# Kernel tuning notes

Measured on AMD Instinct MI355X. Metric: run time of the kernel, lower is better.

## Reference

```python
import jax, jax.numpy as jnp
import numpy as np

N_PANO, N_FP = 50000, 10000
D_IN, D_FP, HID, OUT = 128, 64, 128, 64
E_PP, E_PF = 800000, 50000


def _gat(x_src, x_dst, src, dst, Ws, Wd, a_s, a_d, b, n_dst):
    # PyG GATConv (heads=1, add_self_loops=False, bipartite lin_src/lin_dst)
    hs = x_src @ Ws                      # [Ns, C]
    hd = x_dst @ Wd                      # [Nd, C]
    es = hs @ a_s                        # [Ns]
    ed = hd @ a_d                        # [Nd]
    e = jax.nn.leaky_relu(es[src] + ed[dst], negative_slope=0.2)  # [E]
    m = jax.ops.segment_max(e, dst, num_segments=n_dst)
    ex = jnp.exp(e - m[dst])
    den = jax.ops.segment_sum(ex, dst, num_segments=n_dst)
    alpha = ex / den[dst]                # segment softmax over incoming edges
    out = jax.ops.segment_sum(hs[src] * alpha[:, None], dst, num_segments=n_dst)
    return out + b


def setup_inputs() -> dict:
    key = jax.random.key(0)
    ks = jax.random.split(key, 32)
    s_in = 1.0 / np.sqrt(D_IN)
    s_hid = 1.0 / np.sqrt(HID)
    s_fp = 1.0 / np.sqrt(D_FP)
    inp = {
        "x_pano": jax.random.normal(ks[0], (N_PANO, D_IN), jnp.float32),
        "x_fp": jax.random.normal(ks[1], (N_FP, D_FP), jnp.float32),
        # layer 0 (in = D_IN)
        "Ws0": jax.random.normal(ks[2], (D_IN, HID)) * s_in,
        "Wd0": jax.random.normal(ks[3], (D_IN, HID)) * s_in,
        "as0": jax.random.normal(ks[4], (HID,)) * 0.1,
        "ad0": jax.random.normal(ks[5], (HID,)) * 0.1,
        "b0": jnp.zeros((HID,), jnp.float32),
        "Lw0": jax.random.normal(ks[6], (D_IN, HID)) * s_in,
        "Lb0": jnp.zeros((HID,), jnp.float32),
        # layer 1 (in = HID)
        "Ws1": jax.random.normal(ks[7], (HID, HID)) * s_hid,
        "Wd1": jax.random.normal(ks[8], (HID, HID)) * s_hid,
        "as1": jax.random.normal(ks[9], (HID,)) * 0.1,
        "ad1": jax.random.normal(ks[10], (HID,)) * 0.1,
        "b1": jnp.zeros((HID,), jnp.float32),
        "Lw1": jax.random.normal(ks[11], (HID, HID)) * s_hid,
        "Lb1": jnp.zeros((HID,), jnp.float32),
        # translate conv pano -> footprint
        "Wts": jax.random.normal(ks[12], (HID, OUT)) * s_hid,
        "Wtd": jax.random.normal(ks[13], (D_FP, OUT)) * s_fp,
        "ats": jax.random.normal(ks[14], (OUT,)) * 0.1,
        "atd": jax.random.normal(ks[15], (OUT,)) * 0.1,
        "bt": jnp.zeros((OUT,), jnp.float32),
        "edge_pp": jax.random.randint(ks[16], (2, E_PP), 0, N_PANO),
        "edge_pf_src": jax.random.randint(ks[17], (E_PF,), 0, N_PANO),
        "edge_pf_dst": jax.random.randint(ks[18], (E_PF,), 0, N_FP),
    }
    return inp


def reference(x_pano, x_fp, Ws0, Wd0, as0, ad0, b0, Lw0, Lb0,
              Ws1, Wd1, as1, ad1, b1, Lw1, Lb1,
              Wts, Wtd, ats, atd, bt,
              edge_pp, edge_pf_src, edge_pf_dst):
    src, dst = edge_pp[0], edge_pp[1]
    layer_params = [(Ws0, Wd0, as0, ad0, b0, Lw0, Lb0),
                    (Ws1, Wd1, as1, ad1, b1, Lw1, Lb1)]
    h = x_pano
    for (Ws, Wd, a_s, a_d, b, Lw, Lb) in layer_params:
        conv = _gat(h, h, src, dst, Ws, Wd, a_s, a_d, b, N_PANO)
        h = jax.nn.relu(conv + h @ Lw + Lb)
    # HeteroConv with single relation + aggr='sum' == the bipartite conv output
    out_fp = _gat(h, x_fp, edge_pf_src, edge_pf_dst, Wts, Wtd, ats, atd, bt, N_FP)
    return out_fp
```

## Files before the change

kernel.cpp:

```cpp
#include <hip/hip_runtime.h>
#include <hip/hip_bf16.h>
#include <math.h>

#define N_PANO 50000
#define N_FP   10000
#define N_UNI  60000
#define HID    128
#define OUT_C  64
#define E_PP   800000
#define E_PF   50000
#define E_UNI  850000
#define NBKT   235
#define EPB    4096

typedef unsigned short ushort_t;
typedef unsigned int uint_t;
typedef __attribute__((ext_vector_type(8))) short short8;
typedef __attribute__((ext_vector_type(4))) float f32x4;

static inline int cdiv(int a, int b) { return (a + b - 1) / b; }

__device__ inline ushort_t f2bf(float x) {
    __hip_bfloat16 h = __float2bfloat16(x);
    return *reinterpret_cast<ushort_t*>(&h);
}
__device__ inline float bfu2f(ushort_t u) {
    return __uint_as_float(((uint_t)u) << 16);
}
__device__ inline float bflo(uint_t u) { return __uint_as_float((u & 0xffffu) << 16); }
__device__ inline float bfhi(uint_t u) { return __uint_as_float(u & 0xffff0000u); }
__device__ inline f32x4 mfma16(short8 a, short8 b, f32x4 c) {
    return __builtin_amdgcn_mfma_f32_16x16x32_bf16(a, b, c, 0, 0, 0);
}

__global__ __launch_bounds__(256) void zero_i32(int* p, int n) {
    int i = blockIdx.x * 256 + threadIdx.x;
    if (i < n) p[i] = 0;
}

__global__ __launch_bounds__(256) void bucket_count(const int* __restrict__ pp_dst,
                                                    const int* __restrict__ pf_dst,
                                                    int* __restrict__ bcnt) {
    __shared__ int hist[NBKT];
    const int tid = threadIdx.x;
    const int e0 = blockIdx.x * EPB;
    for (int t = tid; t < NBKT; t += 256) hist[t] = 0;
    __syncthreads();
    #pragma unroll
    for (int u = 0; u < EPB / 256; ++u) {
        int e = e0 + u * 256 + tid;
        int d = -1;
        if (e < E_PP) d = pp_dst[e];
        else if (e < E_UNI) d = N_PANO + pf_dst[e - E_PP];
        if (d >= 0) atomicAdd(&hist[d >> 8], 1);
    }
    __syncthreads();
    for (int t = tid; t < NBKT; t += 256)
        if (hist[t] > 0) atomicAdd(&bcnt[t * 16], hist[t]);
}

__global__ __launch_bounds__(256) void bucket_scan(const int* __restrict__ bcnt,
                                                   int* __restrict__ base, int* __restrict__ bcur) {
    __shared__ int wsum[4];
    int tid = threadIdx.x, lane = tid & 63, wid = tid >> 6;
    int v = (tid < NBKT) ? bcnt[tid * 16] : 0;
    int incl = v;
    #pragma unroll
    for (int off = 1; off < 64; off <<= 1) {
        int t = __shfl_up(incl, off, 64);
        if (lane >= off) incl += t;
    }
    if (lane == 63) wsum[wid] = incl;
    __syncthreads();
    if (tid == 0) {
        int run = 0;
        #pragma unroll
        for (int w = 0; w < 4; ++w) { int t = wsum[w]; wsum[w] = run; run += t; }
    }
    __syncthreads();
    int excl = wsum[wid] + incl - v;
    if (tid < NBKT) { base[tid] = excl; bcur[tid * 16] = excl; }
    if (tid == NBKT) base[NBKT] = E_UNI;
}

__global__ __launch_bounds__(256) void bucket_scatter_uni(const int* __restrict__ pp_src,
                                                          const int* __restrict__ pp_dst,
                                                          const int* __restrict__ pf_src,
                                                          const int* __restrict__ pf_dst,
                                                          int* __restrict__ bcur, int2* __restrict__ tmp) {
    __shared__ int hist[NBKT];
    __shared__ int base[NBKT];
    const int tid = threadIdx.x;
    const int e0 = blockIdx.x * EPB;
    for (int t = tid; t < NBKT; t += 256) hist[t] = 0;
    __syncthreads();
    int d[16], s[16];
    #pragma unroll
    for (int u = 0; u < 16; ++u) {
        int e = e0 + u * 256 + tid;
        if (e < E_PP)       { d[u] = pp_dst[e];                 s[u] = pp_src[e]; }
        else if (e < E_UNI) { d[u] = N_PANO + pf_dst[e - E_PP]; s[u] = pf_src[e - E_PP]; }
        else d[u] = -1;
        if (d[u] >= 0) atomicAdd(&hist[d[u] >> 8], 1);
    }
    __syncthreads();
    for (int t = tid; t < NBKT; t += 256) {
        int c = hist[t];
        base[t] = (c > 0) ? atomicAdd(&bcur[t * 16], c) : 0;
        hist[t] = 0;
    }
    __syncthreads();
    #pragma unroll
    for (int u = 0; u < 16; ++u) {
        if (d[u] >= 0) {
            int b = d[u] >> 8;
            int p = base[b] + atomicAdd(&hist[b], 1);
            tmp[p] = make_int2(s[u], d[u]);
        }
    }
}

__global__ __launch_bounds__(256) void bucket_fine_sort(const int2* __restrict__ tmp,
                                                        const int* __restrict__ base,
                                                        int* __restrict__ ptr, int* __restrict__ col) {
    __shared__ int hist[256];
    __shared__ int wsum[4];
    const int b = blockIdx.x, tid = threadIdx.x, lane = tid & 63, wid = tid >> 6;
    const int B0 = base[b], B1 = base[b + 1];
    hist[tid] = 0;
    __syncthreads();
    for (int e = B0 + tid; e < B1; e += 256) atomicAdd(&hist[tmp[e].y & 255], 1);
    __syncthreads();
    int v = hist[tid];
    int incl = v;
    #pragma unroll
    for (int off = 1; off < 64; off <<= 1) {
        int t = __shfl_up(incl, off, 64);
        if (lane >= off) incl += t;
    }
    if (lane == 63) wsum[wid] = incl;
    __syncthreads();
    if (tid == 0) {
        int run = 0;
        #pragma unroll
        for (int w = 0; w < 4; ++w) { int t = wsum[w]; wsum[w] = run; run += t; }
    }
    __syncthreads();
    int excl = wsum[wid] + incl - v;
    int dg = b * 256 + tid;
    if (dg < N_UNI) ptr[dg] = B0 + excl;
    if (b == NBKT - 1 && tid == 0) ptr[N_UNI] = E_UNI;
    hist[tid] = excl;
    __syncthreads();
    for (int e = B0 + tid; e < B1; e += 256) {
        int2 ed = tmp[e];
        int p = B0 + atomicAdd(&hist[ed.y & 255], 1);
        col[p] = ed.x;
    }
}

__global__ __launch_bounds__(256) void prep_k(const float* __restrict__ Ws0, const float* __restrict__ Lw0,
                                              const float* __restrict__ Ws1, const float* __restrict__ Lw1,
                                              const float* __restrict__ Wts,
                                              const float* __restrict__ Wd0, const float* __restrict__ ad0,
                                              const float* __restrict__ Wd1, const float* __restrict__ ad1,
                                              const float* __restrict__ Wtd, const float* __restrict__ atd,
                                              ushort_t* s0, ushort_t* l0, ushort_t* s1, ushort_t* l1,
                                              ushort_t* ts,
                                              float* wed0, float* wed1, float* wedt) {
    const int blk = blockIdx.x, tid = threadIdx.x;
    if (blk < 288) {
        int i = blk * 256 + tid;
        const float* W; ushort_t* oh;
        int d, NIc, Cc;
        if (i < 65536) {
            int m = i >> 14; d = i & 16383;
            W = (m == 0) ? Ws0 : (m == 1) ? Lw0 : (m == 2) ? Ws1 : Lw1;
            oh = (m == 0) ? s0 : (m == 1) ? l0 : (m == 2) ? s1 : l1;
            NIc = 8; Cc = 128;
        } else if (i < 73728) {
            d = i - 65536; W = Wts; oh = ts;
            NIc = 4; Cc = 64;
        } else return;
        int j = d & 7, l = (d >> 3) & 63;
        int kcl = (d >> 9) & 1;
        int ni = (d >> 10) & (NIc - 1);
        int p = d >> (10 + (NIc == 8 ? 3 : 2));
        int kc = p * 2 + kcl;
        int n = ni * 16 + (l & 15);
        int k = kc * 32 + (l >> 4) * 8 + j;
        oh[d] = f2bf(W[k * Cc + n]);
    } else {
        int r = (blk - 288) * 4 + (tid >> 6);
        int lane = tid & 63;
        const float* W; const float* a; float* o; int rr, C;
        if (r < 128)      { W = Wd0; a = ad0; o = wed0; rr = r;       C = 128; }
        else if (r < 256) { W = Wd1; a = ad1; o = wed1; rr = r - 128; C = 128; }
        else if (r < 320) { W = Wtd; a = atd; o = wedt; rr = r - 256; C = 64;  }
        else return;
        float s = 0.f;
        for (int j = lane; j < C; j += 64) s += W[rr * C + j] * a[j];
        #pragma unroll
        for (int off = 32; off; off >>= 1) s += __shfl_down(s, off, 64);
        if (lane == 0) o[rr] = s;
    }
}

template <int CN, bool DUAL, bool FP32IN>
__global__ __launch_bounds__(256, 2) void gemm_mfma(const float* __restrict__ Xf,
                                                 const ushort_t* __restrict__ Xh,
                                                 const ushort_t* __restrict__ W1, const ushort_t* __restrict__ W2,
                                                 ushort_t* __restrict__ Y1, ushort_t* __restrict__ Y2,
                                                 const float* __restrict__ avec, float* __restrict__ evec,
                                                 const float* __restrict__ wed, float* __restrict__ edv,
                                                 int N) {
    constexpr int NI = CN / 16;
    constexpr int NMAT = DUAL ? 2 : 1;
    constexpr int SLAB = NI * 1024;
    __shared__ ushort_t Bsh[NMAT * SLAB];
    const int tid = threadIdx.x;
    const int w = tid >> 6, l = tid & 63;
    const int col = l & 15, q = l >> 4;
    const int row0 = blockIdx.x * 128 + w * 32;
    f32x4 acc1[2][NI];
    f32x4 acc2[2][DUAL ? NI : 1];
    #pragma unroll
    for (int m = 0; m < 2; ++m)
        #pragma unroll
        for (int ni = 0; ni < NI; ++ni)
            #pragma unroll
            for (int r = 0; r < 4; ++r) acc1[m][ni][r] = 0.f;
    if (DUAL) {
        #pragma unroll
        for (int m = 0; m < 2; ++m)
            #pragma unroll
            for (int ni = 0; ni < NI; ++ni)
                #pragma unroll
                for (int r = 0; r < 4; ++r) acc2[m][ni][r] = 0.f;
    }
    float ped[2] = {0.f, 0.f};

    #pragma unroll
    for (int p = 0; p < 2; ++p) {
        if (p) __syncthreads();
        {
            const uint4* src1 = (const uint4*)W1 + p * (SLAB / 8);
            uint4* dst1 = (uint4*)&Bsh[0];
            #pragma unroll
            for (int f = tid; f < SLAB / 8; f += 256) dst1[f] = src1[f];
            if (DUAL) {
                const uint4* src2 = (const uint4*)W2 + p * (SLAB / 8);
                uint4* dst2 = (uint4*)&Bsh[SLAB];
                #pragma unroll
                for (int f = tid; f < SLAB / 8; f += 256) dst2[f] = src2[f];
            }
        }
        __syncthreads();
        #pragma unroll
        for (int kcl = 0; kcl < 2; ++kcl) {
            const int kc = p * 2 + kcl;
            const int k0 = kc * 32 + q * 8;
            short8 Ah[2];
            #pragma unroll
            for (int m = 0; m < 2; ++m) {
                const int arow = row0 + m * 16 + col;
                if (FP32IN) {
                    float xv[8];
                    if (arow < N) {
                        float4 a0 = *(const float4*)&Xf[(size_t)arow * 128 + k0];
                        float4 a1 = *(const float4*)&Xf[(size_t)arow * 128 + k0 + 4];
                        xv[0] = a0.x; xv[1] = a0.y; xv[2] = a0.z; xv[3] = a0.w;
                        xv[4] = a1.x; xv[5] = a1.y; xv[6] = a1.z; xv[7] = a1.w;
                    } else {
                        #pragma unroll
                        for (int j = 0; j < 8; ++j) xv[j] = 0.f;
                    }
                    #pragma unroll
                    for (int j = 0; j < 8; ++j) Ah[m][j] = (short)f2bf(xv[j]);
                    if (wed) {
                        float4 w0 = *(const float4*)&wed[k0];
                        float4 w1 = *(const float4*)&wed[k0 + 4];
                        ped[m] += xv[0] * w0.x + xv[1] * w0.y + xv[2] * w0.z + xv[3] * w0.w
                                + xv[4] * w1.x + xv[5] * w1.y + xv[6] * w1.z + xv[7] * w1.w;
                    }
                } else {
                    if (arow < N) {
                        Ah[m] = *(const short8*)&Xh[(size_t)arow * 128 + k0];
                    } else {
                        #pragma unroll
                        for (int j = 0; j < 8; ++j) Ah[m][j] = 0;
                    }
                    if (wed) {
                        float4 w0 = *(const float4*)&wed[k0];
                        float4 w1 = *(const float4*)&wed[k0 + 4];
                        float wv[8] = {w0.x, w0.y, w0.z, w0.w, w1.x, w1.y, w1.z, w1.w};
                        #pragma unroll
                        for (int j = 0; j < 8; ++j)
                            ped[m] += bfu2f((ushort_t)Ah[m][j]) * wv[j];
                    }
                }
            }
            #pragma unroll
            for (int ni = 0; ni < NI; ++ni) {
                const int lb = ((ni * 2 + kcl) * 64 + l) * 8;
                short8 B1 = *(const short8*)&Bsh[lb];
                #pragma unroll
                for (int m = 0; m < 2; ++m) acc1[m][ni] = mfma16(Ah[m], B1, acc1[m][ni]);
                if (DUAL) {
                    short8 B2 = *(const short8*)&Bsh[SLAB + lb];
                    #pragma unroll
                    for (int m = 0; m < 2; ++m) acc2[m][ni] = mfma16(Ah[m], B2, acc2[m][ni]);
                }
            }
        }
    }

    #pragma unroll
    for (int m = 0; m < 2; ++m) {
        #pragma unroll
        for (int ni = 0; ni < NI; ++ni) {
            #pragma unroll
            for (int r = 0; r < 4; ++r) {
                int mrow = row0 + m * 16 + q * 4 + r;
                if (mrow < N) {
                    Y1[(size_t)mrow * CN + ni * 16 + col] = f2bf(acc1[m][ni][r]);
                    if (DUAL) Y2[(size_t)mrow * CN + ni * 16 + col] = f2bf(acc2[m][ni][r]);
                }
            }
        }
    }
    float av[NI];
    #pragma unroll
    for (int ni = 0; ni < NI; ++ni) av[ni] = avec[ni * 16 + col];
    #pragma unroll
    for (int m = 0; m < 2; ++m) {
        #pragma unroll
        for (int r = 0; r < 4; ++r) {
            float pp = 0.f;
            #pragma unroll
            for (int ni = 0; ni < NI; ++ni) pp += acc1[m][ni][r] * av[ni];
            pp += __shfl_xor(pp, 1, 64);
            pp += __shfl_xor(pp, 2, 64);
            pp += __shfl_xor(pp, 4, 64);
            pp += __shfl_xor(pp, 8, 64);
            int mrow = row0 + m * 16 + q * 4 + r;
            if (col == 0 && mrow < N) evec[mrow] = pp;
        }
    }
    if (wed) {
        #pragma unroll
        for (int m = 0; m < 2; ++m) {
            ped[m] += __shfl_xor(ped[m], 16, 64);
            ped[m] += __shfl_xor(ped[m], 32, 64);
            int arow = row0 + m * 16 + col;
            if (q == 0 && arow < N) edv[arow] = ped[m];
        }
    }
}

__global__ __launch_bounds__(256) void agg_pano7(const int* __restrict__ ptr, const int* __restrict__ col,
                                                 const float* __restrict__ es, const float* __restrict__ ed,
                                                 const ushort_t* __restrict__ hsb, const ushort_t* __restrict__ linb,
                                                 const float* __restrict__ b, const float* __restrict__ Lb,
                                                 uint_t* __restrict__ hh, int N) {
    int lane = threadIdx.x & 63, wid = threadIdx.x >> 6;
    int nodeA = blockIdx.x * 8 + wid * 2;
    if (nodeA >= N) return;
    int nodeB = nodeA + 1;
    bool hasB = nodeB < N;
    int begA = ptr[nodeA], endA = ptr[nodeA + 1];
    int endB = hasB ? ptr[nodeB + 1] : endA;
    int begB = endA;
    float ednA = ed[nodeA];
    float ednB = hasB ? ed[nodeB] : 0.f;
    const int half = lane >> 5, hl = lane & 31;
    float aA0 = 0.f, aA1 = 0.f, aA2 = 0.f, aA3 = 0.f, dA = 0.f;
    float aB0 = 0.f, aB1 = 0.f, aB2 = 0.f, aB3 = 0.f, dB = 0.f;
    int baseA = begA, baseB = begB;
    while (baseA < endA || baseB < endB) {
        int mA = endA - baseA; mA = mA < 0 ? 0 : (mA > 64 ? 64 : mA);
        int mB = endB - baseB; mB = mB < 0 ? 0 : (mB > 64 ? 64 : mB);
        int sA = 0, sB = 0;
        float wA = 0.f, wB = 0.f;
        if (lane < mA) {
            sA = col[baseA + lane];
            float e = es[sA] + ednA;
            e = fmaxf(e, 0.2f * e);
            wA = __expf(e);
        }
        if (lane < mB) {
            sB = col[baseB + lane];
            float e = es[sB] + ednB;
            e = fmaxf(e, 0.2f * e);
            wB = __expf(e);
        }
        dA += wA; dB += wB;
        {
            int mp = (mA + 1) & ~1;
            int t = 0;
            for (; t + 8 <= mp; t += 8) {
                int i0 = t + half, i1 = t + 2 + half, i2 = t + 4 + half, i3 = t + 6 + half;
                int s0 = __shfl(sA, i0, 64), s1 = __shfl(sA, i1, 64);
                int s2 = __shfl(sA, i2, 64), s3 = __shfl(sA, i3, 64);
                float w0 = __shfl(wA, i0, 64), w1 = __shfl(wA, i1, 64);
                float w2 = __shfl(wA, i2, 64), w3 = __shfl(wA, i3, 64);
                uint2 h0 = *(const uint2*)&hsb[(size_t)s0 * 128 + hl * 4];
                uint2 h1 = *(const uint2*)&hsb[(size_t)s1 * 128 + hl * 4];
                uint2 h2 = *(const uint2*)&hsb[(size_t)s2 * 128 + hl * 4];
                uint2 h3 = *(const uint2*)&hsb[(size_t)s3 * 128 + hl * 4];
                aA0 += w0 * bflo(h0.x) + w1 * bflo(h1.x) + w2 * bflo(h2.x) + w3 * bflo(h3.x);
                aA1 += w0 * bfhi(h0.x) + w1 * bfhi(h1.x) + w2 * bfhi(h2.x) + w3 * bfhi(h3.x);
                aA2 += w0 * bflo(h0.y) + w1 * bflo(h1.y) + w2 * bflo(h2.y) + w3 * bflo(h3.y);
                aA3 += w0 * bfhi(h0.y) + w1 * bfhi(h1.y) + w2 * bfhi(h2.y) + w3 * bfhi(h3.y);
            }
            for (; t < mp; t += 2) {
                int i0 = t + half;
                int s0 = __shfl(sA, i0, 64);
                float w0 = __shfl(wA, i0, 64);
                uint2 h0 = *(const uint2*)&hsb[(size_t)s0 * 128 + hl * 4];
                aA0 += w0 * bflo(h0.x);
                aA1 += w0 * bfhi(h0.x);
                aA2 += w0 * bflo(h0.y);
                aA3 += w0 * bfhi(h0.y);
            }
        }
        {
            int mp = (mB + 1) & ~1;
            int t = 0;
            for (; t + 8 <= mp; t += 8) {
                int i0 = t + half, i1 = t + 2 + half, i2 = t + 4 + half, i3 = t + 6 + half;
                int s0 = __shfl(sB, i0, 64), s1 = __shfl(sB, i1, 64);
                int s2 = __shfl(sB, i2, 64), s3 = __shfl(sB, i3, 64);
                float w0 = __shfl(wB, i0, 64), w1 = __shfl(wB, i1, 64);
                float w2 = __shfl(wB, i2, 64), w3 = __shfl(wB, i3, 64);
                uint2 h0 = *(const uint2*)&hsb[(size_t)s0 * 128 + hl * 4];
                uint2 h1 = *(const uint2*)&hsb[(size_t)s1 * 128 + hl * 4];
                uint2 h2 = *(const uint2*)&hsb[(size_t)s2 * 128 + hl * 4];
                uint2 h3 = *(const uint2*)&hsb[(size_t)s3 * 128 + hl * 4];
                aB0 += w0 * bflo(h0.x) + w1 * bflo(h1.x) + w2 * bflo(h2.x) + w3 * bflo(h3.x);
                aB1 += w0 * bfhi(h0.x) + w1 * bfhi(h1.x) + w2 * bfhi(h2.x) + w3 * bfhi(h3.x);
                aB2 += w0 * bflo(h0.y) + w1 * bflo(h1.y) + w2 * bflo(h2.y) + w3 * bflo(h3.y);
                aB3 += w0 * bfhi(h0.y) + w1 * bfhi(h1.y) + w2 * bfhi(h2.y) + w3 * bfhi(h3.y);
            }
            for (; t < mp; t += 2) {
                int i0 = t + half;
                int s0 = __shfl(sB, i0, 64);
                float w0 = __shfl(wB, i0, 64);
                uint2 h0 = *(const uint2*)&hsb[(size_t)s0 * 128 + hl * 4];
                aB0 += w0 * bflo(h0.x);
                aB1 += w0 * bfhi(h0.x);
                aB2 += w0 * bflo(h0.y);
                aB3 += w0 * bfhi(h0.y);
            }
        }
        baseA += 64; baseB += 64;
    }
    aA0 += __shfl_xor(aA0, 32, 64); aA1 += __shfl_xor(aA1, 32, 64);
    aA2 += __shfl_xor(aA2, 32, 64); aA3 += __shfl_xor(aA3, 32, 64);
    aB0 += __shfl_xor(aB0, 32, 64); aB1 += __shfl_xor(aB1, 32, 64);
    aB2 += __shfl_xor(aB2, 32, 64); aB3 += __shfl_xor(aB3, 32, 64);
    #pragma unroll
    for (int off = 1; off < 64; off <<= 1) dA += __shfl_xor(dA, off, 64);
    #pragma unroll
    for (int off = 1; off < 64; off <<= 1) dB += __shfl_xor(dB, off, 64);
    float invA = (endA > begA) ? (1.f / dA) : 0.f;
    float invB = (endB > begB) ? (1.f / dB) : 0.f;
    int node = half ? nodeB : nodeA;
    if (half == 0 || hasB) {
        float v0 = half ? aB0 : aA0, v1 = half ? aB1 : aA1;
        float v2 = half ? aB2 : aA2, v3 = half ? aB3 : aA3;
        float inv = half ? invB : invA;
        uint2 lv = *(const uint2*)&linb[(size_t)node * 128 + hl * 4];
        float4 bb = *(const float4*)&b[hl * 4];
        float4 lb4 = *(const float4*)&Lb[hl * 4];
        float o0 = fmaxf(v0 * inv + bb.x + bflo(lv.x) + lb4.x, 0.f);
        float o1 = fmaxf(v1 * inv + bb.y + bfhi(lv.x) + lb4.y, 0.f);
        float o2 = fmaxf(v2 * inv + bb.z + bflo(lv.y) + lb4.z, 0.f);
        float o3 = fmaxf(v3 * inv + bb.w + bfhi(lv.y) + lb4.w, 0.f);
        uint2 ov;
        ov.x = (uint_t)f2bf(o0) | ((uint_t)f2bf(o1) << 16);
        ov.y = (uint_t)f2bf(o2) | ((uint_t)f2bf(o3) << 16);
        *(uint2*)&hh[(size_t)node * 64 + hl * 2] = ov;
    }
}

__global__ __launch_bounds__(256) void agg_fp5(const int* __restrict__ ptr, const int* __restrict__ col,
                                               const float* __restrict__ es, const float* __restrict__ x_fp,
                                               const float* __restrict__ wedt,
                                               const ushort_t* __restrict__ hsb, const float* __restrict__ bt,
                                               float* __restrict__ out, int N) {
    int lane = threadIdx.x & 63, wid = threadIdx.x >> 6;
    int node = blockIdx.x * 4 + wid;
    if (node >= N) return;
    int beg = ptr[node], end = ptr[node + 1];
    float edn = x_fp[(size_t)node * 64 + lane] * wedt[lane];
    #pragma unroll
    for (int off = 1; off < 64; off <<= 1) edn += __shfl_xor(edn, off, 64);
    float acc = 0.f, denp = 0.f;
    for (int base = beg; base < end; base += 64) {
        int m = min(64, end - base);
        int s = 0;
        float wgt = 0.f;
        if (lane < m) {
            s = col[base + lane];
            float e = es[s] + edn;
            e = fmaxf(e, 0.2f * e);
            wgt = __expf(e);
        }
        denp += wgt;
        int u = 0;
        for (; u + 4 <= m; u += 4) {
            int s0 = __shfl(s, u, 64), s1 = __shfl(s, u + 1, 64);
            int s2 = __shfl(s, u + 2, 64), s3 = __shfl(s, u + 3, 64);
            float w0 = __shfl(wgt, u, 64), w1 = __shfl(wgt, u + 1, 64);
            float w2 = __shfl(wgt, u + 2, 64), w3 = __shfl(wgt, u + 3, 64);
            float h0 = bfu2f(hsb[(size_t)s0 * 64 + lane]);
            float h1 = bfu2f(hsb[(size_t)s1 * 64 + lane]);
            float h2 = bfu2f(hsb[(size_t)s2 * 64 + lane]);
            float h3 = bfu2f(hsb[(size_t)s3 * 64 + lane]);
            acc += w0 * h0 + w1 * h1 + w2 * h2 + w3 * h3;
        }
        for (; u < m; ++u) {
            int su = __shfl(s, u, 64);
            float wu = __shfl(wgt, u, 64);
            acc += wu * bfu2f(hsb[(size_t)su * 64 + lane]);
        }
    }
    float den = denp;
    #pragma unroll
    for (int off = 1; off < 64; off <<= 1) den += __shfl_xor(den, off, 64);
    float inv = (end > beg) ? (1.f / den) : 0.f;
    out[(size_t)node * 64 + lane] = acc * inv + bt[lane];
}

extern "C" void kernel_launch(void* const* d_in, const int* in_sizes, int n_in,
                              void* d_out, int out_size, void* d_ws, size_t ws_size,
                              hipStream_t stream) {
    const float* x_pano = (const float*)d_in[0];
    const float* x_fp   = (const float*)d_in[1];
    const float* Ws0 = (const float*)d_in[2];
    const float* Wd0 = (const float*)d_in[3];
    const float* as0 = (const float*)d_in[4];
    const float* ad0 = (const float*)d_in[5];
    const float* b0  = (const float*)d_in[6];
    const float* Lw0 = (const float*)d_in[7];
    const float* Lb0 = (const float*)d_in[8];
    const float* Ws1 = (const float*)d_in[9];
    const float* Wd1 = (const float*)d_in[10];
    const float* as1 = (const float*)d_in[11];
    const float* ad1 = (const float*)d_in[12];
    const float* b1  = (const float*)d_in[13];
    const float* Lw1 = (const float*)d_in[14];
    const float* Lb1 = (const float*)d_in[15];
    const float* Wts = (const float*)d_in[16];
    const float* Wtd = (const float*)d_in[17];
    const float* ats = (const float*)d_in[18];
    const float* atd = (const float*)d_in[19];
    const float* bt  = (const float*)d_in[20];
    const int* edge_pp = (const int*)d_in[21];
    const int* pf_src  = (const int*)d_in[22];
    const int* pf_dst  = (const int*)d_in[23];
    float* out = (float*)d_out;

    char* wsp = (char*)d_ws;
    size_t off = 0;
    auto alloc = [&](size_t bytes) -> char* {
        char* p = wsp + off;
        off += (bytes + 255) & ~(size_t)255;
        return p;
    };
    ushort_t* hsb  = (ushort_t*)alloc(sizeof(ushort_t) * N_PANO * HID);
    ushort_t* linb = (ushort_t*)alloc(sizeof(ushort_t) * N_PANO * HID);
    uint_t* hh     = (uint_t*)alloc(sizeof(uint_t) * N_PANO * 64);
    ushort_t* hstb = (ushort_t*)alloc(sizeof(ushort_t) * N_PANO * OUT_C);
    int2* tmp_e    = (int2*)alloc(sizeof(int2) * E_UNI);
    float* es   = (float*)alloc(sizeof(float) * N_PANO);
    float* ed   = (float*)alloc(sizeof(float) * N_PANO);
    float* wed0 = (float*)alloc(sizeof(float) * HID);
    float* wed1 = (float*)alloc(sizeof(float) * HID);
    float* wedt = (float*)alloc(sizeof(float) * OUT_C);
    ushort_t* s0 = (ushort_t*)alloc(sizeof(ushort_t) * 128 * 128);
    ushort_t* l0 = (ushort_t*)alloc(sizeof(ushort_t) * 128 * 128);
    ushort_t* s1 = (ushort_t*)alloc(sizeof(ushort_t) * 128 * 128);
    ushort_t* l1 = (ushort_t*)alloc(sizeof(ushort_t) * 128 * 128);
    ushort_t* ts = (ushort_t*)alloc(sizeof(ushort_t) * 64 * 128);
    int* bcnt   = (int*)alloc(sizeof(int) * NBKT * 16);
    int* bcur   = (int*)alloc(sizeof(int) * NBKT * 16);
    int* bbase  = (int*)alloc(sizeof(int) * (NBKT + 1));
    int* P      = (int*)alloc(sizeof(int) * (N_UNI + 1));
    int* col_u  = (int*)alloc(sizeof(int) * E_UNI);

    const int* pp_src = edge_pp;
    const int* pp_dst = edge_pp + E_PP;

    zero_i32<<<cdiv(NBKT * 16, 256), 256, 0, stream>>>(bcnt, NBKT * 16);
    bucket_count<<<cdiv(E_UNI, EPB), 256, 0, stream>>>(pp_dst, pf_dst, bcnt);
    bucket_scan<<<1, 256, 0, stream>>>(bcnt, bbase, bcur);
    bucket_scatter_uni<<<cdiv(E_UNI, EPB), 256, 0, stream>>>(pp_src, pp_dst, pf_src, pf_dst, bcur, tmp_e);
    bucket_fine_sort<<<NBKT, 256, 0, stream>>>(tmp_e, bbase, P, col_u);

    prep_k<<<368, 256, 0, stream>>>(Ws0, Lw0, Ws1, Lw1, Wts, Wd0, ad0, Wd1, ad1, Wtd, atd,
                                    s0, l0, s1, l1, ts, wed0, wed1, wedt);

    const int gemm_grid = cdiv(N_PANO, 128);

    gemm_mfma<128, true, true><<<gemm_grid, 256, 0, stream>>>(
        x_pano, nullptr, s0, l0, hsb, linb, as0, es, wed0, ed, N_PANO);
    agg_pano7<<<cdiv(N_PANO, 8), 256, 0, stream>>>(P, col_u, es, ed, hsb, linb, b0, Lb0, hh, N_PANO);

    gemm_mfma<128, true, false><<<gemm_grid, 256, 0, stream>>>(
        nullptr, (const ushort_t*)hh, s1, l1, hsb, linb, as1, es, wed1, ed, N_PANO);
    agg_pano7<<<cdiv(N_PANO, 8), 256, 0, stream>>>(P, col_u, es, ed, hsb, linb, b1, Lb1, hh, N_PANO);

    gemm_mfma<64, false, false><<<gemm_grid, 256, 0, stream>>>(
        nullptr, (const ushort_t*)hh, ts, nullptr, hstb, nullptr, ats, es, nullptr, nullptr, N_PANO);
    agg_fp5<<<cdiv(N_FP, 4), 256, 0, stream>>>(P + N_PANO, col_u, es, x_fp, wedt, hstb, bt, out, N_FP);
}
```

Before: 277.8 us.

## Replace atomic bucket sort with per-tile counts, scan, and fused weight prep

Removes the zero kernel and the global atomic bucket cursors. Each edge tile now writes its per-bucket histogram to a tile-major count matrix, a per-bucket scan computes exclusive offsets, and the scatter places edges at fixed positions without global atomics. Weight conversion prep is folded into the count kernel launch. This cuts kernel launches from six to four, removes global atomic contention, and makes the coarse ordering deterministic. In exchange, the scatter re-scans bucket totals in every block.

Result: faster. 267.4 us (-3.7%).

```diff
diff --git a/kernel.cpp b/kernel.cpp
--- a/kernel.cpp
+++ b/kernel.cpp
@@ -12,6 +12,7 @@
 #define E_UNI  850000
 #define NBKT   235
 #define EPB    4096
+#define NT_CNT 208
 
 typedef unsigned short ushort_t;
 typedef unsigned int uint_t;
@@ -33,144 +34,35 @@
     return __builtin_amdgcn_mfma_f32_16x16x32_bf16(a, b, c, 0, 0, 0);
 }
 
-__global__ __launch_bounds__(256) void zero_i32(int* p, int n) {
-    int i = blockIdx.x * 256 + threadIdx.x;
-    if (i < n) p[i] = 0;
-}
-
-__global__ __launch_bounds__(256) void bucket_count(const int* __restrict__ pp_dst,
-                                                    const int* __restrict__ pf_dst,
-                                                    int* __restrict__ bcnt) {
+__global__ __launch_bounds__(256) void csr_count_prep(
+        const int* __restrict__ pp_dst, const int* __restrict__ pf_dst,
+        int* __restrict__ pcnt,
+        const float* __restrict__ Ws0, const float* __restrict__ Lw0,
+        const float* __restrict__ Ws1, const float* __restrict__ Lw1,
+        const float* __restrict__ Wts,
+        const float* __restrict__ Wd0, const float* __restrict__ ad0,
+        const float* __restrict__ Wd1, const float* __restrict__ ad1,
+        const float* __restrict__ Wtd, const float* __restrict__ atd,
+        ushort_t* s0, ushort_t* l0, ushort_t* s1, ushort_t* l1, ushort_t* ts,
+        float* wed0, float* wed1, float* wedt) {
     __shared__ int hist[NBKT];
-    const int tid = threadIdx.x;
-    const int e0 = blockIdx.x * EPB;
-    for (int t = tid; t < NBKT; t += 256) hist[t] = 0;
-    __syncthreads();
-    #pragma unroll
-    for (int u = 0; u < EPB / 256; ++u) {
-        int e = e0 + u * 256 + tid;
-        int d = -1;
-        if (e < E_PP) d = pp_dst[e];
-        else if (e < E_UNI) d = N_PANO + pf_dst[e - E_PP];
-        if (d >= 0) atomicAdd(&hist[d >> 8], 1);
-    }
-    __syncthreads();
-    for (int t = tid; t < NBKT; t += 256)
-        if (hist[t] > 0) atomicAdd(&bcnt[t * 16], hist[t]);
-}
-
-__global__ __launch_bounds__(256) void bucket_scan(const int* __restrict__ bcnt,
-                                                   int* __restrict__ base, int* __restrict__ bcur) {
-    __shared__ int wsum[4];
-    int tid = threadIdx.x, lane = tid & 63, wid = tid >> 6;
-    int v = (tid < NBKT) ? bcnt[tid * 16] : 0;
-    int incl = v;
-    #pragma unroll
-    for (int off = 1; off < 64; off <<= 1) {
-        int t = __shfl_up(incl, off, 64);
-        if (lane >= off) incl += t;
-    }
-    if (lane == 63) wsum[wid] = incl;
-    __syncthreads();
-    if (tid == 0) {
-        int run = 0;
-        #pragma unroll
-        for (int w = 0; w < 4; ++w) { int t = wsum[w]; wsum[w] = run; run += t; }
-    }
-    __syncthreads();
-    int excl = wsum[wid] + incl - v;
-    if (tid < NBKT) { base[tid] = excl; bcur[tid * 16] = excl; }
-    if (tid == NBKT) base[NBKT] = E_UNI;
-}
-
-__global__ __launch_bounds__(256) void bucket_scatter_uni(const int* __restrict__ pp_src,
-                                                          const int* __restrict__ pp_dst,
-                                                          const int* __restrict__ pf_src,
-                                                          const int* __restrict__ pf_dst,
-                                                          int* __restrict__ bcur, int2* __restrict__ tmp) {
-    __shared__ int hist[NBKT];
-    __shared__ int base[NBKT];
-    const int tid = threadIdx.x;
-    const int e0 = blockIdx.x * EPB;
-    for (int t = tid; t < NBKT; t += 256) hist[t] = 0;
-    __syncthreads();
-    int d[16], s[16];
-    #pragma unroll
-    for (int u = 0; u < 16; ++u) {
-        int e = e0 + u * 256 + tid;
-        if (e < E_PP)       { d[u] = pp_dst[e];                 s[u] = pp_src[e]; }
-        else if (e < E_UNI) { d[u] = N_PANO + pf_dst[e - E_PP]; s[u] = pf_src[e - E_PP]; }
-        else d[u] = -1;
-        if (d[u] >= 0) atomicAdd(&hist[d[u] >> 8], 1);
-    }
-    __syncthreads();
-    for (int t = tid; t < NBKT; t += 256) {
-        int c = hist[t];
-        base[t] = (c > 0) ? atomicAdd(&bcur[t * 16], c) : 0;
-        hist[t] = 0;
-    }
-    __syncthreads();
-    #pragma unroll
-    for (int u = 0; u < 16; ++u) {
-        if (d[u] >= 0) {
-            int b = d[u] >> 8;
-            int p = base[b] + atomicAdd(&hist[b], 1);
-            tmp[p] = make_int2(s[u], d[u]);
-        }
-    }
-}
-
-__global__ __launch_bounds__(256) void bucket_fine_sort(const int2* __restrict__ tmp,
-                                                        const int* __restrict__ base,
-                                                        int* __restrict__ ptr, int* __restrict__ col) {
-    __shared__ int hist[256];
-    __shared__ int wsum[4];
-    const int b = blockIdx.x, tid = threadIdx.x, lane = tid & 63, wid = tid >> 6;
-    const int B0 = base[b], B1 = base[b + 1];
-    hist[tid] = 0;
-    __syncthreads();
-    for (int e = B0 + tid; e < B1; e += 256) atomicAdd(&hist[tmp[e].y & 255], 1);
-    __syncthreads();
-    int v = hist[tid];
-    int incl = v;
-    #pragma unroll
-    for (int off = 1; off < 64; off <<= 1) {
-        int t = __shfl_up(incl, off, 64);
-        if (lane >= off) incl += t;
-    }
-    if (lane == 63) wsum[wid] = incl;
-    __syncthreads();
-    if (tid == 0) {
-        int run = 0;
-        #pragma unroll
-        for (int w = 0; w < 4; ++w) { int t = wsum[w]; wsum[w] = run; run += t; }
-    }
-    __syncthreads();
-    int excl = wsum[wid] + incl - v;
-    int dg = b * 256 + tid;
-    if (dg < N_UNI) ptr[dg] = B0 + excl;
-    if (b == NBKT - 1 && tid == 0) ptr[N_UNI] = E_UNI;
-    hist[tid] = excl;
-    __syncthreads();
-    for (int e = B0 + tid; e < B1; e += 256) {
-        int2 ed = tmp[e];
-        int p = B0 + atomicAdd(&hist[ed.y & 255], 1);
-        col[p] = ed.x;
-    }
-}
-
-__global__ __launch_bounds__(256) void prep_k(const float* __restrict__ Ws0, const float* __restrict__ Lw0,
-                                              const float* __restrict__ Ws1, const float* __restrict__ Lw1,
-                                              const float* __restrict__ Wts,
-                                              const float* __restrict__ Wd0, const float* __restrict__ ad0,
-                                              const float* __restrict__ Wd1, const float* __restrict__ ad1,
-                                              const float* __restrict__ Wtd, const float* __restrict__ atd,
-                                              ushort_t* s0, ushort_t* l0, ushort_t* s1, ushort_t* l1,
-                                              ushort_t* ts,
-                                              float* wed0, float* wed1, float* wedt) {
-    const int blk = blockIdx.x, tid = threadIdx.x;
-    if (blk < 288) {
-        int i = blk * 256 + tid;
+    const int tile = blockIdx.x, tid = threadIdx.x;
+    if (tile < NT_CNT) {
+        for (int t = tid; t < NBKT; t += 256) hist[t] = 0;
+        __syncthreads();
+        const int e0 = tile * EPB;
+        #pragma unroll
+        for (int u = 0; u < 16; ++u) {
+            int e = e0 + u * 256 + tid;
+            int d = -1;
+            if (e < E_PP) d = pp_dst[e];
+            else if (e < E_UNI) d = N_PANO + pf_dst[e - E_PP];
+            if (d >= 0) atomicAdd(&hist[d >> 8], 1);
+        }
+        __syncthreads();
+        for (int t = tid; t < NBKT; t += 256) pcnt[t * NT_CNT + tile] = hist[t];
+    } else if (tile < NT_CNT + 288) {
+        int i = (tile - NT_CNT) * 256 + tid;
         const float* W; ushort_t* oh;
         int d, NIc, Cc;
         if (i < 65536) {
@@ -191,7 +83,7 @@
         int k = kc * 32 + (l >> 4) * 8 + j;
         oh[d] = f2bf(W[k * Cc + n]);
     } else {
-        int r = (blk - 288) * 4 + (tid >> 6);
+        int r = (tile - NT_CNT - 288) * 4 + (tid >> 6);
         int lane = tid & 63;
         const float* W; const float* a; float* o; int rr, C;
         if (r < 128)      { W = Wd0; a = ad0; o = wed0; rr = r;       C = 128; }
@@ -203,6 +95,119 @@
         #pragma unroll
         for (int off = 32; off; off >>= 1) s += __shfl_down(s, off, 64);
         if (lane == 0) o[rr] = s;
+    }
+}
+
+__global__ __launch_bounds__(256) void csr_scan(const int* __restrict__ pcnt,
+                                                int* __restrict__ pexc, int* __restrict__ btot) {
+    __shared__ int wsum[4];
+    const int b = blockIdx.x, tid = threadIdx.x, lane = tid & 63, wv = tid >> 6;
+    int v = (tid < NT_CNT) ? pcnt[b * NT_CNT + tid] : 0;
+    int incl = v;
+    #pragma unroll
+    for (int off = 1; off < 64; off <<= 1) {
+        int t = __shfl_up(incl, off, 64);
+        if (lane >= off) incl += t;
+    }
+    if (lane == 63) wsum[wv] = incl;
+    __syncthreads();
+    if (tid == 0) {
+        int run = 0;
+        #pragma unroll
+        for (int w = 0; w < 4; ++w) { int t = wsum[w]; wsum[w] = run; run += t; }
+    }
+    __syncthreads();
+    int excl = wsum[wv] + incl - v;
+    if (tid < NT_CNT) pexc[b * NT_CNT + tid] = excl;
+    if (tid == 255) btot[b] = excl;
+}
+
+__global__ __launch_bounds__(256) void csr_scatter(const int* __restrict__ pp_src,
+                                                   const int* __restrict__ pp_dst,
+                                                   const int* __restrict__ pf_src,
+                                                   const int* __restrict__ pf_dst,
+                                                   const int* __restrict__ pexc,
+                                                   const int* __restrict__ btot,
+                                                   int* __restrict__ bbase_out,
+                                                   int2* __restrict__ tmp) {
+    __shared__ int base2[NBKT];
+    __shared__ int cur[NBKT];
+    __shared__ int wsum[4];
+    const int tile = blockIdx.x, tid = threadIdx.x, lane = tid & 63, wv = tid >> 6;
+    int v = (tid < NBKT) ? btot[tid] : 0;
+    int incl = v;
+    #pragma unroll
+    for (int off = 1; off < 64; off <<= 1) {
+        int t = __shfl_up(incl, off, 64);
+        if (lane >= off) incl += t;
+    }
+    if (lane == 63) wsum[wv] = incl;
+    __syncthreads();
+    if (tid == 0) {
+        int run = 0;
+        #pragma unroll
+        for (int w = 0; w < 4; ++w) { int t = wsum[w]; wsum[w] = run; run += t; }
+    }
+    __syncthreads();
+    int excl = wsum[wv] + incl - v;
+    if (tid < NBKT) {
+        base2[tid] = excl + pexc[tid * NT_CNT + tile];
+        cur[tid] = 0;
+        if (tile == 0) bbase_out[tid] = excl;
+    }
+    if (tile == 0 && tid == 0) bbase_out[NBKT] = E_UNI;
+    __syncthreads();
+    const int e0 = tile * EPB;
+    #pragma unroll
+    for (int u = 0; u < 16; ++u) {
+        int e = e0 + u * 256 + tid;
+        int d = -1, s = 0;
+        if (e < E_PP)       { d = pp_dst[e];                 s = pp_src[e]; }
+        else if (e < E_UNI) { d = N_PANO + pf_dst[e - E_PP]; s = pf_src[e - E_PP]; }
+        if (d >= 0) {
+            int b = d >> 8;
+            int p = base2[b] + atomicAdd(&cur[b], 1);
+            tmp[p] = make_int2(s, d);
+        }
+    }
+}
+
+__global__ __launch_bounds__(256) void csr_sort(const int2* __restrict__ tmp,
+                                                const int* __restrict__ bbase,
+                                                int* __restrict__ ptr, int* __restrict__ col) {
+    __shared__ int hist[256];
+    __shared__ int wsum[4];
+    const int b = blockIdx.x, tid = threadIdx.x, lane = tid & 63, wv = tid >> 6;
+    const int B0 = bbase[b], B1 = bbase[b + 1];
+    hist[tid] = 0;
+    __syncthreads();
+    for (int e = B0 + tid; e < B1; e += 256) atomicAdd(&hist[tmp[e].y & 255], 1);
+    __syncthreads();
+    int v = hist[tid];
+    int incl = v;
+    #pragma unroll
+    for (int off = 1; off < 64; off <<= 1) {
+        int t = __shfl_up(incl, off, 64);
+        if (lane >= off) incl += t;
+    }
+    if (lane == 63) wsum[wv] = incl;
+    __syncthreads();
+    if (tid == 0) {
+        int run = 0;
+        #pragma unroll
+        for (int w = 0; w < 4; ++w) { int t = wsum[w]; wsum[w] = run; run += t; }
+    }
+    __syncthreads();
+    int excl = wsum[wv] + incl - v;
+    int dg = b * 256 + tid;
+    if (dg < N_UNI) ptr[dg] = B0 + excl;
+    if (b == NBKT - 1 && tid == 0) ptr[N_UNI] = E_UNI;
+    hist[tid] = excl;
+    __syncthreads();
+    for (int e = B0 + tid; e < B1; e += 256) {
+        int2 ed2 = tmp[e];
+        int p = B0 + atomicAdd(&hist[ed2.y & 255], 1);
+        col[p] = ed2.x;
     }
 }
 
@@ -557,9 +562,10 @@
     const float* ats = (const float*)d_in[18];
     const float* atd = (const float*)d_in[19];
     const float* bt  = (const float*)d_in[20];
-    const int* edge_pp = (const int*)d_in[21];
-    const int* pf_src  = (const int*)d_in[22];
-    const int* pf_dst  = (const int*)d_in[23];
+    const int* pp_src = (const int*)d_in[21];
+    const int* pp_dst = (const int*)d_in[21] + E_PP;
+    const int* pf_src = (const int*)d_in[22];
+    const int* pf_dst = (const int*)d_in[23];
     float* out = (float*)d_out;
 
     char* wsp = (char*)d_ws;
@@ -584,23 +590,19 @@
     ushort_t* s1 = (ushort_t*)alloc(sizeof(ushort_t) * 128 * 128);
     ushort_t* l1 = (ushort_t*)alloc(sizeof(ushort_t) * 128 * 128);
     ushort_t* ts = (ushort_t*)alloc(sizeof(ushort_t) * 64 * 128);
-    int* bcnt   = (int*)alloc(sizeof(int) * NBKT * 16);
-    int* bcur   = (int*)alloc(sizeof(int) * NBKT * 16);
-    int* bbase  = (int*)alloc(sizeof(int) * (NBKT + 1));
-    int* P      = (int*)alloc(sizeof(int) * (N_UNI + 1));
-    int* col_u  = (int*)alloc(sizeof(int) * E_UNI);
-
-    const int* pp_src = edge_pp;
-    const int* pp_dst = edge_pp + E_PP;
-
-    zero_i32<<<cdiv(NBKT * 16, 256), 256, 0, stream>>>(bcnt, NBKT * 16);
-    bucket_count<<<cdiv(E_UNI, EPB), 256, 0, stream>>>(pp_dst, pf_dst, bcnt);
-    bucket_scan<<<1, 256, 0, stream>>>(bcnt, bbase, bcur);
-    bucket_scatter_uni<<<cdiv(E_UNI, EPB), 256, 0, stream>>>(pp_src, pp_dst, pf_src, pf_dst, bcur, tmp_e);
-    bucket_fine_sort<<<NBKT, 256, 0, stream>>>(tmp_e, bbase, P, col_u);
-
-    prep_k<<<368, 256, 0, stream>>>(Ws0, Lw0, Ws1, Lw1, Wts, Wd0, ad0, Wd1, ad1, Wtd, atd,
-                                    s0, l0, s1, l1, ts, wed0, wed1, wedt);
+    int* pcnt  = (int*)alloc(sizeof(int) * NBKT * NT_CNT);
+    int* pexc  = (int*)alloc(sizeof(int) * NBKT * NT_CNT);
+    int* btot  = (int*)alloc(sizeof(int) * NBKT);
+    int* bbase = (int*)alloc(sizeof(int) * (NBKT + 1));
+    int* P     = (int*)alloc(sizeof(int) * (N_UNI + 1));
+    int* col_u = (int*)alloc(sizeof(int) * E_UNI);
+
+    csr_count_prep<<<NT_CNT + 288 + 80, 256, 0, stream>>>(
+        pp_dst, pf_dst, pcnt, Ws0, Lw0, Ws1, Lw1, Wts,
+        Wd0, ad0, Wd1, ad1, Wtd, atd, s0, l0, s1, l1, ts, wed0, wed1, wedt);
+    csr_scan<<<NBKT, 256, 0, stream>>>(pcnt, pexc, btot);
+    csr_scatter<<<NT_CNT, 256, 0, stream>>>(pp_src, pp_dst, pf_src, pf_dst, pexc, btot, bbase, tmp_e);
+    csr_sort<<<NBKT, 256, 0, stream>>>(tmp_e, bbase, P, col_u);
 
     const int gemm_grid = cdiv(N_PANO, 128);
 
```
